# Kernel tuning notes

Measured on AMD Instinct MI355X. Metric: run time of the kernel, lower is better.

The kernel has to match this reference:

```python
import jax, jax.numpy as jnp
import numpy as np

D_MODEL = 1024
N_HEADS = 16
D_HEAD = D_MODEL // N_HEADS
B, T = 2, 2048


def setup_inputs() -> dict:
    key = jax.random.key(0)
    ks = jax.random.split(key, 8)
    s = 1.0 / np.sqrt(D_MODEL)
    return {
        "x": jax.random.normal(ks[0], (B, T, D_MODEL), dtype=jnp.float32),
        "ln_g": jnp.ones((D_MODEL,), jnp.float32),
        "ln_b": jnp.zeros((D_MODEL,), jnp.float32),
        "w_qkv": jax.random.normal(ks[1], (D_MODEL, 3 * D_MODEL), jnp.float32) * s,
        "b_qkv": jnp.zeros((3 * D_MODEL,), jnp.float32),
        "w_gate": jax.random.normal(ks[2], (D_MODEL, D_MODEL), jnp.float32) * s,
        "b_gate": jnp.zeros((D_MODEL,), jnp.float32),
        "w_proj": jax.random.normal(ks[3], (D_MODEL, D_MODEL), jnp.float32) * s,
        "b_proj": jnp.zeros((D_MODEL,), jnp.float32),
    }


def reference(x, ln_g, ln_b, w_qkv, b_qkv, w_gate, b_gate, w_proj, b_proj):
    Bb, Tt, Dd = x.shape
    H, dh = N_HEADS, D_HEAD

    # LayerNorm (eps=1e-5, torch default)
    mu = jnp.mean(x, axis=-1, keepdims=True)
    var = jnp.mean((x - mu) ** 2, axis=-1, keepdims=True)
    x_norm = (x - mu) / jnp.sqrt(var + 1e-5) * ln_g + ln_b

    qkv = x_norm @ w_qkv + b_qkv
    q, k, v = jnp.split(qkv, 3, axis=-1)

    # concept gate on the RAW input x (not x_norm), normalized by its mean
    gate_sig = jax.nn.sigmoid(x @ w_gate + b_gate)
    gate_norm = gate_sig / (jnp.mean(gate_sig, axis=-1, keepdims=True) + 1e-5)
    q = q * gate_norm
    k = k * gate_norm

    # [B,T,D] -> [B,H,T,dh]
    def to_heads(t):
        return t.reshape(Bb, Tt, H, dh).transpose(0, 2, 1, 3)

    q, k, v = to_heads(q), to_heads(k), to_heads(v)

    q = jax.nn.elu(q) + 1.0
    k = jax.nn.elu(k) + 1.0

    # materialized outer-product cumsum (faithful to source formulation)
    kv = jnp.einsum("bhtd,bhtm->bhtdm", k, v)          # [B,H,T,dh,dh]
    kv_cumsum = jnp.cumsum(kv, axis=2)
    out_num = jnp.einsum("bhtd,bhtdm->bhtm", q, kv_cumsum)
    k_cumsum = jnp.cumsum(k, axis=2)
    out_den = jnp.einsum("bhtd,bhtd->bht", q, k_cumsum)[..., None] + 1e-5
    out = out_num / out_den                              # [B,H,T,dh]

    out = out.transpose(0, 2, 1, 3).reshape(Bb, Tt, Dd)
    return out @ w_proj + b_proj
```

## Files before the change

### kernel.cpp

```cpp
#include <hip/hip_runtime.h>
#include <math.h>

constexpr int D      = 1024;
constexpr int H      = 16;
constexpr int DH     = 64;
constexpr int Bb     = 2;
constexpr int T      = 2048;
constexpr int BT     = Bb * T;
constexpr int CHUNK  = 64;
constexpr int NC     = T / CHUNK;
constexpr int LS     = 72;

typedef __attribute__((ext_vector_type(8))) short bf16x8;
typedef __attribute__((ext_vector_type(4))) float f32x4;

#define GLOAD_LDS16(gp, lp) \
    __builtin_amdgcn_global_load_lds((const __attribute__((address_space(1))) void*)(gp), \
                                     (__attribute__((address_space(3))) void*)(lp), 16, 0, 0)

__device__ __forceinline__ short to_bf16(float f) {
    unsigned u = __float_as_uint(f);
    unsigned r = (u + 0x7fffu + ((u >> 16) & 1u)) >> 16;
    return (short)r;
}
__device__ __forceinline__ float bf2f(short s) {
    return __uint_as_float(((unsigned)(unsigned short)s) << 16);
}

__device__ __forceinline__ float elu1(float x) {
    return x > 0.0f ? x + 1.0f : __expf(x);
}

__global__ __launch_bounds__(256) void pre_kernel(const float* __restrict__ x,
                                                  const float* __restrict__ g,
                                                  const float* __restrict__ b,
                                                  const float* __restrict__ wq,
                                                  const float* __restrict__ wg,
                                                  const float* __restrict__ wp,
                                                  short* __restrict__ ynb,
                                                  short* __restrict__ xbb,
                                                  short* __restrict__ wTcomb,
                                                  short* __restrict__ wTp,
                                                  float* __restrict__ gmean) {
    __shared__ short tile[32][33];
    int bid = blockIdx.x;
    if (bid < 1024) {
        int row  = bid * 4 + (threadIdx.x >> 6);
        int lane = threadIdx.x & 63;
        const float* xr = x + (size_t)row * D;
        float4 xv[4];
        float s = 0.0f;
        #pragma unroll
        for (int i = 0; i < 4; ++i) {
            xv[i] = *(const float4*)(xr + i * 256 + lane * 4);
            s += xv[i].x + xv[i].y + xv[i].z + xv[i].w;
        }
        #pragma unroll
        for (int off = 32; off > 0; off >>= 1) s += __shfl_xor(s, off, 64);
        float mu = s * (1.0f / D);
        float vs = 0.0f;
        #pragma unroll
        for (int i = 0; i < 4; ++i) {
            float d0 = xv[i].x - mu, d1 = xv[i].y - mu;
            float d2 = xv[i].z - mu, d3 = xv[i].w - mu;
            vs += d0 * d0 + d1 * d1 + d2 * d2 + d3 * d3;
        }
        #pragma unroll
        for (int off = 32; off > 0; off >>= 1) vs += __shfl_xor(vs, off, 64);
        float rstd = rsqrtf(vs * (1.0f / D) + 1e-5f);
        if (lane == 0) gmean[row] = 0.0f;
        #pragma unroll
        for (int i = 0; i < 4; ++i) {
            int cc = i * 256 + lane * 4;
            float4 gv = *(const float4*)(g + cc);
            float4 bv = *(const float4*)(b + cc);
            short4 o, xo;
            o.x = to_bf16((xv[i].x - mu) * rstd * gv.x + bv.x);
            o.y = to_bf16((xv[i].y - mu) * rstd * gv.y + bv.y);
            o.z = to_bf16((xv[i].z - mu) * rstd * gv.z + bv.z);
            o.w = to_bf16((xv[i].w - mu) * rstd * gv.w + bv.w);
            xo.x = to_bf16(xv[i].x); xo.y = to_bf16(xv[i].y);
            xo.z = to_bf16(xv[i].z); xo.w = to_bf16(xv[i].w);
            *(short4*)(ynb + (size_t)row * D + cc) = o;
            *(short4*)(xbb + (size_t)row * D + cc) = xo;
        }
    } else {
        int t2 = bid - 1024;
        const float* W; short* Wt; int N; int t;
        if (t2 < 3072)      { W = wq; Wt = wTcomb;                       N = 3072; t = t2; }
        else if (t2 < 4096) { W = wg; Wt = wTcomb + (size_t)3072 * 1024; N = 1024; t = t2 - 3072; }
        else                { W = wp; Wt = wTp;                          N = 1024; t = t2 - 4096; }
        int ntiles = N >> 5;
        int nb = (t % ntiles) * 32, kb = (t / ntiles) * 32;
        int tx = threadIdx.x & 31, ty = threadIdx.x >> 5;
        #pragma unroll
        for (int i = 0; i < 4; ++i) {
            int k = kb + ty + i * 8;
            tile[ty + i * 8][tx] = to_bf16(W[(size_t)k * N + nb + tx]);
        }
        __syncthreads();
        #pragma unroll
        for (int i = 0; i < 4; ++i) {
            int n = nb + ty + i * 8;
            Wt[(size_t)n * 1024 + kb + tx] = tile[tx][ty + i * 8];
        }
    }
}

#define SWZ(os) ((os) ^ ((((os) >> 6) & 3) << 3))
#define BARX() __builtin_amdgcn_s_barrier()
#define LGKM0() asm volatile("s_waitcnt lgkmcnt(0)" ::: "memory")
#define VMW(n) asm volatile("s_waitcnt vmcnt(" #n ")" ::: "memory")
#define MEMFENCE() asm volatile("" ::: "memory")

#define STG(Mp, rb, t, kc, isB) do {                                                       \
    short* _b = ldsbuf + ((((t) & 1)) << 15) + (((((isB) << 1) | (kc))) << 13) + wid * 1024; \
    const short* _g = (Mp) + (size_t)((rb) + wid * 32 + s_r) * 1024 + (t) * 64 + (kc) * 32 + s_c; \
    GLOAD_LDS16(_g, _b);                                                                   \
    GLOAD_LDS16(_g + (size_t)16 * 1024, _b + 512);                                         \
} while (0)

#define FRAGA(t, kc, mi) (*(const bf16x8*)(ldsbuf + (((t) & 1) << 15) + ((kc) << 13) + \
    SWZ((wm * 128 + (mi) * 16 + fr) * 32 + fk)))
#define FRAGB(t, kc, ni) (*(const bf16x8*)(ldsbuf + (((t) & 1) << 15) + ((2 + (kc)) << 13) + \
    SWZ((wn * 64 + (ni) * 16 + fr) * 32 + fk)))

#define GROUP(t, S1, S2, S3, S4, W2, W4) do {                                              \
    bf16x8 af[8], bq[4];                                                                   \
    _Pragma("unroll") for (int mi = 0; mi < 8; ++mi) af[mi] = FRAGA(t, 0, mi);             \
// ... 49 lines not shown
                                                             short* __restrict__ sigb,
                                                             float* __restrict__ gmean) {
    __shared__ short ldsbuf[2 * 32768];

    const int bid   = blockIdx.x;
    const int xcd   = bid & 7;
    const int local = bid >> 3;
    const int cx = xcd & 3, ry = xcd >> 2;
    const int bxx = cx * 4 + (local & 3);
    const int byy = ry * 8 + (local >> 2);
    const int row0 = byy * 256;
    const int col0 = bxx * 256;
    const bool isg = (col0 >= 3 * D);
    const short* Ap = isg ? xb : xnb;

    const int tid  = threadIdx.x;
    const int wid  = tid >> 6;
    const int lane = tid & 63;
    const int wm = wid >> 2;
    const int wn = wid & 3;
    const int fr = lane & 15;
    const int fk = (lane >> 4) * 8;

    const int s_r = lane >> 2;
    const int s_c = 8 * ((lane & 3) ^ ((lane >> 3) & 3));

    f32x4 acc[8][4] = {};

    STG(Ap, row0, 0, 0, 0); MEMFENCE();
    STG(Wt, col0, 0, 0, 1); MEMFENCE();
    STG(Ap, row0, 0, 1, 0); MEMFENCE();
    STG(Wt, col0, 0, 1, 1); MEMFENCE();
    STG(Ap, row0, 1, 0, 0); MEMFENCE();
    STG(Wt, col0, 1, 0, 1); MEMFENCE();
    STG(Ap, row0, 1, 1, 0);
    VMW(10);
    BARX();

    for (int t = 0; t < 14; ++t) GROUP(t, 1, 1, 1, 1, VMW(10), VMW(10));
    GROUP(14, 1, 0, 0, 0, VMW(8), VMW(4));
    GROUP(15, 0, 0, 0, 0, VMW(0), (void)0);

    const int ccol  = lane & 15;
    const int crow4 = (lane >> 4) * 4;
    if (!isg) {
        #pragma unroll
        for (int mi = 0; mi < 8; ++mi) {
            #pragma unroll
            for (int ni = 0; ni < 4; ++ni) {
                int col = col0 + wn * 64 + ni * 16 + ccol;
                float bv = b_qkv[col];
                #pragma unroll
                for (int r = 0; r < 4; ++r) {
                    int row = row0 + wm * 128 + mi * 16 + crow4 + r;
                    qkvb[(size_t)row * (3 * D) + col] = to_bf16(acc[mi][ni][r] + bv);
                }
            }
        }
    } else {
        #pragma unroll
        for (int mi = 0; mi < 8; ++mi) {
            #pragma unroll
            for (int r = 0; r < 4; ++r) {
                int lrow = row0 + wm * 128 + mi * 16 + crow4 + r;
                float psum = 0.0f;
                #pragma unroll
                for (int ni = 0; ni < 4; ++ni) {
                    int col = col0 + wn * 64 + ni * 16 + ccol - 3 * D;
                    float v = acc[mi][ni][r] + b_gate[col];
                    float sv = 1.0f / (1.0f + __expf(-v));
                    sigb[(size_t)lrow * D + col] = to_bf16(sv);
                    psum += sv;
                }
                psum += __shfl_xor(psum, 1, 64);
                psum += __shfl_xor(psum, 2, 64);
                psum += __shfl_xor(psum, 4, 64);
                psum += __shfl_xor(psum, 8, 64);
                if (ccol == 0) atomicAdd(&gmean[lrow], psum);
            }
        }
    }
}

__global__ __launch_bounds__(256) void chunk_state_mfma(const short* __restrict__ qkvb,
                                                        const short* __restrict__ sigb,
                                                        const float* __restrict__ gmean,
                                                        float* __restrict__ Sc,
                                                        float* __restrict__ zc) {
    __shared__ short Kt[DH * LS];
    __shared__ short Vt[DH * LS];
    int idx = blockIdx.x;
    int c = idx & (NC - 1), h = (idx >> 5) & (H - 1), b = idx >> 9;
    size_t bt0 = (size_t)b * T + c * CHUNK;
    const short* kbase = qkvb + bt0 * (3 * D) + D + h * DH;
    const short* vbase = kbase + D;
    const short* sbase = sigb + bt0 * D + h * DH;
    int tid = threadIdx.x;

    #pragma unroll
    for (int l = 0; l < 2; ++l) {
        int i  = tid + l * 256;
        int t  = i >> 3;
        int d8 = (i & 7) * 8;
        float invm = 1.0f / (gmean[bt0 + t] * (1.0f / D) + 1e-5f);
        bf16x8 kv = *(const bf16x8*)(kbase + (size_t)t * (3 * D) + d8);
        bf16x8 vv = *(const bf16x8*)(vbase + (size_t)t * (3 * D) + d8);
        bf16x8 sg = *(const bf16x8*)(sbase + (size_t)t * D + d8);
        #pragma unroll
        for (int j = 0; j < 8; ++j) {
            float gn = bf2f(sg[j]) * invm;
            Kt[(d8 + j) * LS + t] = to_bf16(elu1(bf2f(kv[j]) * gn));
            Vt[(d8 + j) * LS + t] = vv[j];
        }
    }
    __syncthreads();

    const int wv = tid >> 6, lane = tid & 63;
    const int fr = lane & 15, quad = lane >> 4;
    const int fk = quad * 8, crow4 = quad * 4, ccol = lane & 15;
    const int mbase = wv * 16;

    bf16x8 af[2];
    af[0] = *(const bf16x8*)&Vt[(mbase + fr) * LS + fk];
    af[1] = *(const bf16x8*)&Vt[(mbase + fr) * LS + 32 + fk];

    f32x4 acc[4] = {};
    #pragma unroll
    for (int n = 0; n < 4; ++n) {
        #pragma unroll
        for (int ck = 0; ck < 2; ++ck) {
            bf16x8 bk = *(const bf16x8*)&Kt[(n * 16 + fr) * LS + ck * 32 + fk];
            acc[n] = __builtin_amdgcn_mfma_f32_16x16x32_bf16(af[ck], bk, acc[n], 0, 0, 0);
        }
    }

    float* Sd = Sc + (size_t)idx * (DH * DH);
    #pragma unroll
    for (int n = 0; n < 4; ++n)
        #pragma unroll
        for (int r = 0; r < 4; ++r)
            Sd[(mbase + crow4 + r) * DH + n * 16 + ccol] = acc[n][r];

    {
        int d = tid >> 2, p = tid & 3;
        bf16x8 k0 = *(const bf16x8*)&Kt[d * LS + p * 16];
        bf16x8 k1 = *(const bf16x8*)&Kt[d * LS + p * 16 + 8];
        float zs = 0.0f;
        #pragma unroll
        for (int j = 0; j < 8; ++j) zs += bf2f(k0[j]) + bf2f(k1[j]);
        zs += __shfl_xor(zs, 1, 64);
        zs += __shfl_xor(zs, 2, 64);
        if (p == 0) zc[(size_t)idx * DH + d] = zs;
    }
}

__global__ __launch_bounds__(256) void chunk_prefix_kernel(const float* __restrict__ S,
                                                           short* __restrict__ Spb,
                                                           float* __restrict__ z) {
    int bh   = blockIdx.x >> 4;
    int part = blockIdx.x & 15;
    int e    = part * 256 + threadIdx.x;
    const float* Sb = S + (size_t)bh * NC * DH * DH;
    short* Pb = Spb + (size_t)bh * NC * DH * DH;
    float v[NC];
    #pragma unroll
    for (int c = 0; c < NC; ++c) v[c] = Sb[(size_t)c * DH * DH + e];
    float acc = 0.0f;
    #pragma unroll
    for (int c = 0; c < NC; ++c) {
        Pb[(size_t)c * DH * DH + e] = to_bf16(acc);
        acc += v[c];
    }
    if (part == 0 && threadIdx.x < DH) {
        float* zb = z + (size_t)bh * NC * DH + threadIdx.x;
        float zv[NC];
        #pragma unroll
        for (int c = 0; c < NC; ++c) zv[c] = zb[(size_t)c * DH];
        float za = 0.0f;
        #pragma unroll
        for (int c = 0; c < NC; ++c) {
            zb[(size_t)c * DH] = za;
            za += zv[c];
        }
    }
}

__global__ __launch_bounds__(256) void chunk_attn_mfma(const short* __restrict__ qkvb,
                                                       const short* __restrict__ sigb,
                                                       const float* __restrict__ gmean,
                                                       const short* __restrict__ Spb,
                                                       const float* __restrict__ zc,
                                                       short* __restrict__ attnb) {
    __shared__ short Qs[CHUNK * LS];
    __shared__ short Ks[CHUNK * LS];
    __shared__ short Vt[DH * LS];
    __shared__ short Ss[DH * LS];
    __shared__ float zpL[DH];
    __shared__ float den[CHUNK];
    short* As = Ks;

    int idx = blockIdx.x;
    int c = idx & (NC - 1), h = (idx >> 5) & (H - 1), b = idx >> 9;
    size_t bt0 = (size_t)b * T + c * CHUNK;
    const short* qbase = qkvb + bt0 * (3 * D) + h * DH;
    const short* kbase = qbase + D;
    const short* vbase = qbase + 2 * D;
    const short* sbase = sigb + bt0 * D + h * DH;
    const short* spb = Spb + (size_t)idx * (DH * DH);
    int tid = threadIdx.x;

    #pragma unroll
    for (int l = 0; l < 2; ++l) {
        int i  = tid + l * 256;
        int t  = i >> 3;
        int d8 = (i & 7) * 8;
        float invm = 1.0f / (gmean[bt0 + t] * (1.0f / D) + 1e-5f);
        bf16x8 qv = *(const bf16x8*)(qbase + (size_t)t * (3 * D) + d8);
        bf16x8 kv = *(const bf16x8*)(kbase + (size_t)t * (3 * D) + d8);
        bf16x8 vv = *(const bf16x8*)(vbase + (size_t)t * (3 * D) + d8);
        bf16x8 sg = *(const bf16x8*)(sbase + (size_t)t * D + d8);
        bf16x8 qg, kg;
        #pragma unroll
        for (int j = 0; j < 8; ++j) {
            float gn = bf2f(sg[j]) * invm;
            qg[j] = to_bf16(elu1(bf2f(qv[j]) * gn));
            kg[j] = to_bf16(elu1(bf2f(kv[j]) * gn));
            Vt[(d8 + j) * LS + t] = vv[j];
        }
        *(bf16x8*)&Qs[t * LS + d8] = qg;
        *(bf16x8*)&Ks[t * LS + d8] = kg;
        *(bf16x8*)&Ss[t * LS + d8] = *(const bf16x8*)(spb + (size_t)i * 8);
    }
    if (tid < DH) zpL[tid] = zc[(size_t)idx * DH + tid];
    __syncthreads();

    const int wv = tid >> 6, lane = tid & 63;
    const int fr = lane & 15, quad = lane >> 4;
    const int fk = quad * 8, crow4 = quad * 4, ccol = lane & 15;
    const int tbase = wv * 16;

    bf16x8 aq[2];
    aq[0] = *(const bf16x8*)&Qs[(tbase + fr) * LS + fk];
    aq[1] = *(const bf16x8*)&Qs[(tbase + fr) * LS + 32 + fk];

    f32x4 accs[4] = {};
    #pragma unroll
    for (int n = 0; n < 4; ++n) {
        #pragma unroll
        for (int ck = 0; ck < 2; ++ck) {
            bf16x8 bk = *(const bf16x8*)&Ks[(n * 16 + fr) * LS + ck * 32 + fk];
            accs[n] = __builtin_amdgcn_mfma_f32_16x16x32_bf16(aq[ck], bk, accs[n], 0, 0, 0);
        }
    }
    __syncthreads();

    float part[4] = {0.f, 0.f, 0.f, 0.f};
    #pragma unroll
    for (int n = 0; n < 4; ++n) {
        #pragma unroll
        for (int r = 0; r < 4; ++r) {
            int tt = tbase + crow4 + r;
            int ss = n * 16 + ccol;
            float v = (ss <= tt) ? accs[n][r] : 0.0f;
            part[r] += v;
            As[tt * LS + ss] = to_bf16(v);
        }
    }
    #pragma unroll
    for (int r = 0; r < 4; ++r) {
        part[r] += __shfl_xor(part[r], 1, 64);
        part[r] += __shfl_xor(part[r], 2, 64);
        part[r] += __shfl_xor(part[r], 4, 64);
        part[r] += __shfl_xor(part[r], 8, 64);
    }
    if (fr == 0) {
        #pragma unroll
        for (int r = 0; r < 4; ++r) den[tbase + crow4 + r] = part[r];
    }
    __syncthreads();

    {
        int t = tid >> 2, p = tid & 3;
        bf16x8 q0 = *(const bf16x8*)&Qs[t * LS + p * 16];
        bf16x8 q1 = *(const bf16x8*)&Qs[t * LS + p * 16 + 8];
        float qz = 0.0f;
        #pragma unroll
        for (int j = 0; j < 8; ++j)
            qz += bf2f(q0[j]) * zpL[p * 16 + j] + bf2f(q1[j]) * zpL[p * 16 + 8 + j];
        qz += __shfl_xor(qz, 1, 64);
        qz += __shfl_xor(qz, 2, 64);
        if (p == 0) den[t] += qz + 1e-5f;
    }

    f32x4 acco[4] = {};
    #pragma unroll
    for (int m4 = 0; m4 < 4; ++m4) {
        #pragma unroll
        for (int ck = 0; ck < 2; ++ck) {
            bf16x8 bs = *(const bf16x8*)&Ss[(m4 * 16 + fr) * LS + ck * 32 + fk];
            acco[m4] = __builtin_amdgcn_mfma_f32_16x16x32_bf16(aq[ck], bs, acco[m4], 0, 0, 0);
        }
    }
    bf16x8 aa[2];
    aa[0] = *(const bf16x8*)&As[(tbase + fr) * LS + fk];
    aa[1] = *(const bf16x8*)&As[(tbase + fr) * LS + 32 + fk];
    #pragma unroll
    for (int m4 = 0; m4 < 4; ++m4) {
        #pragma unroll
        for (int ck = 0; ck < 2; ++ck) {
            bf16x8 bv = *(const bf16x8*)&Vt[(m4 * 16 + fr) * LS + ck * 32 + fk];
            acco[m4] = __builtin_amdgcn_mfma_f32_16x16x32_bf16(aa[ck], bv, acco[m4], 0, 0, 0);
        }
    }
    __syncthreads();

    short* obase = attnb + bt0 * D + h * DH;
    #pragma unroll
    for (int r = 0; r < 4; ++r) {
        int tt = tbase + crow4 + r;
        float rv = 1.0f / den[tt];
        #pragma unroll
        for (int m4 = 0; m4 < 4; ++m4)
            obase[(size_t)tt * D + m4 * 16 + ccol] = to_bf16(acco[m4][r] * rv);
    }
}

__global__ __launch_bounds__(256) void gemm_proj64(const short* __restrict__ A,
                                                   const short* __restrict__ Bt,
                                                   const float* __restrict__ bias,
                                                   float* __restrict__ C) {
    constexpr int BK = 32, K = 1024, N = 1024;
    __shared__ short Als[64 * BK];
    __shared__ short Bls[128 * BK];

    const int bid   = blockIdx.x;
    const int xcd   = bid & 7;
    const int local = bid >> 3;
    const int cx = xcd & 3, ry = xcd >> 2;
    const int lx = local & 1, ly = local >> 1;
    const int bxx = cx * 2 + lx;
    const int byy = ry * 32 + ly;

    const int tid  = threadIdx.x;
    const int wave = tid >> 6;
    const int lane = tid & 63;
    const int row0 = byy * 64;
    const int col0 = bxx * 128;
    const int wn = wave * 32;

    f32x4 acc[4][2] = {};
    const int srow = lane >> 2;
    const int skk  = (lane & 3) * 8;
    const int fr = lane & 15;
    const int fk = (lane >> 4) * 8;

    for (int k0 = 0; k0 < K; k0 += BK) {
        __syncthreads();
        #pragma unroll
        for (int u = 0; u < 3; ++u) {
            int cc = wave * 3 + u;
            if (cc < 4) {
                int r = cc * 16 + srow;
                GLOAD_LDS16(A + (size_t)(row0 + r) * K + k0 + skk, &Als[cc * 512]);
            } else {
                int c2 = cc - 4;
                int r = c2 * 16 + srow;
                GLOAD_LDS16(Bt + (size_t)(col0 + r) * K + k0 + skk, &Bls[c2 * 512]);
            }
        }
        __syncthreads();

        bf16x8 af[4], bfr[2];
        #pragma unroll
        for (int i = 0; i < 4; ++i)
            af[i] = *(const bf16x8*)&Als[(i * 16 + fr) * BK + fk];
        #pragma unroll
        for (int j = 0; j < 2; ++j)
            bfr[j] = *(const bf16x8*)&Bls[(wn + j * 16 + fr) * BK + fk];
        #pragma unroll
        for (int mi = 0; mi < 4; ++mi)
            #pragma unroll
            for (int ni = 0; ni < 2; ++ni)
                acc[mi][ni] = __builtin_amdgcn_mfma_f32_16x16x32_bf16(af[mi], bfr[ni], acc[mi][ni], 0, 0, 0);
    }

    const int ccol  = lane & 15;
    const int crow4 = (lane >> 4) * 4;
    #pragma unroll
    for (int mi = 0; mi < 4; ++mi) {
        #pragma unroll
        for (int ni = 0; ni < 2; ++ni) {
            int col = col0 + wn + ni * 16 + ccol;
            float bv = bias[col];
            #pragma unroll
            for (int r = 0; r < 4; ++r) {
                int row = row0 + mi * 16 + crow4 + r;
                C[(size_t)row * N + col] = acc[mi][ni][r] + bv;
            }
        }
    }
}

extern "C" void kernel_launch(void* const* d_in, const int* in_sizes, int n_in,
                              void* d_out, int out_size, void* d_ws, size_t ws_size,
                              hipStream_t stream) {
    const float* x      = (const float*)d_in[0];
    const float* ln_g   = (const float*)d_in[1];
    const float* ln_b   = (const float*)d_in[2];
    const float* w_qkv  = (const float*)d_in[3];
    const float* b_qkv  = (const float*)d_in[4];
    const float* w_gate = (const float*)d_in[5];
    const float* b_gate = (const float*)d_in[6];
    const float* w_proj = (const float*)d_in[7];
    const float* b_proj = (const float*)d_in[8];
    float* out = (float*)d_out;

    short* xnb   = (short*)d_ws;
    short* xb    = xnb + (size_t)BT * D;
    short* wTc   = xb + (size_t)BT * D;
    short* wTp   = wTc + (size_t)4096 * 1024;
    short* qkvb  = wTp + (size_t)D * D;
    short* sigb  = qkvb + (size_t)BT * 3 * D;
    short* attnb = sigb + (size_t)BT * D;
    float* zc    = (float*)(attnb + (size_t)BT * D);
    float* gmean = zc + (size_t)Bb * H * NC * DH;
    float* Sc    = (float*)xnb;
    short* Spb   = wTc;

    pre_kernel<<<1024 + 5120, 256, 0, stream>>>(x, ln_g, ln_b, w_qkv, w_gate, w_proj,
                                                xnb, xb, wTc, wTp, gmean);
    gemm_fused_qkvgate<<<256, 512, 0, stream>>>(
        xnb, xb, wTc, b_qkv, b_gate, qkvb, sigb, gmean);
    chunk_state_mfma<<<Bb * H * NC, 256, 0, stream>>>(qkvb, sigb, gmean, Sc, zc);
    chunk_prefix_kernel<<<Bb * H * 16, 256, 0, stream>>>(Sc, Spb, zc);
    chunk_attn_mfma<<<Bb * H * NC, 256, 0, stream>>>(qkvb, sigb, gmean, Spb, zc, attnb);
    gemm_proj64<<<512, 256, 0, stream>>>(attnb, wTp, b_proj, out);
}
```

Before: 190.6 us.

## Fuse chunk state, prefix and attention kernels with software grid barriers

Merges the three chunked linear-attention kernels into one persistent 512-block kernel, with two atomic-counter grid barriers replacing the kernel boundaries. Each block handles two chunks and keeps their transposed V tiles in LDS across the barriers, so V is not reloaded in the attention phase. The aim is to cut two launch gaps and some global traffic. The cost is that all 512 blocks must be co-resident (launch bounds request 3 blocks per CU) or the barrier deadlocks, and LDS use per block grows.

```diff
diff --git a/kernel.cpp b/kernel.cpp
--- a/kernel.cpp
+++ b/kernel.cpp
@@ -29,6 +29,17 @@
 
 __device__ __forceinline__ float elu1(float x) {
     return x > 0.0f ? x + 1.0f : __expf(x);
+}
+
+__device__ __forceinline__ void grid_barrier(unsigned* ctr, unsigned target) {
+    __threadfence();
+    __syncthreads();
+    if (threadIdx.x == 0) {
+        __hip_atomic_fetch_add(ctr, 1u, __ATOMIC_ACQ_REL, __HIP_MEMORY_SCOPE_AGENT);
+        while (__hip_atomic_load(ctr, __ATOMIC_ACQUIRE, __HIP_MEMORY_SCOPE_AGENT) < target)
+            __builtin_amdgcn_s_sleep(2);
+    }
+    __syncthreads();
 }
 
 __global__ __launch_bounds__(256) void pre_kernel(const float* __restrict__ x,
@@ -41,10 +52,12 @@
                                                   short* __restrict__ xbb,
                                                   short* __restrict__ wTcomb,
                                                   short* __restrict__ wTp,
-                                                  float* __restrict__ gmean) {
+                                                  float* __restrict__ gmean,
+                                                  unsigned* __restrict__ ctrs) {
     __shared__ short tile[32][33];
     int bid = blockIdx.x;
     if (bid < 1024) {
+        if (bid == 0 && threadIdx.x < 2) ctrs[threadIdx.x] = 0;
         int row  = bid * 4 + (threadIdx.x >> 6);
         int lane = threadIdx.x & 63;
         const float* xr = x + (size_t)row * D;
@@ -260,246 +273,240 @@
     }
 }
 
-__global__ __launch_bounds__(256) void chunk_state_mfma(const short* __restrict__ qkvb,
-                                                        const short* __restrict__ sigb,
-                                                        const float* __restrict__ gmean,
-                                                        float* __restrict__ Sc,
-                                                        float* __restrict__ zc) {
-    __shared__ short Kt[DH * LS];
-    __shared__ short Vt[DH * LS];
-    int idx = blockIdx.x;
-    int c = idx & (NC - 1), h = (idx >> 5) & (H - 1), b = idx >> 9;
-    size_t bt0 = (size_t)b * T + c * CHUNK;
-    const short* kbase = qkvb + bt0 * (3 * D) + D + h * DH;
-    const short* vbase = kbase + D;
-    const short* sbase = sigb + bt0 * D + h * DH;
-    int tid = threadIdx.x;
-
-    #pragma unroll
-    for (int l = 0; l < 2; ++l) {
-        int i  = tid + l * 256;
-        int t  = i >> 3;
-        int d8 = (i & 7) * 8;
-        float invm = 1.0f / (gmean[bt0 + t] * (1.0f / D) + 1e-5f);
-        bf16x8 kv = *(const bf16x8*)(kbase + (size_t)t * (3 * D) + d8);
-        bf16x8 vv = *(const bf16x8*)(vbase + (size_t)t * (3 * D) + d8);
-        bf16x8 sg = *(const bf16x8*)(sbase + (size_t)t * D + d8);
-        #pragma unroll
-        for (int j = 0; j < 8; ++j) {
-            float gn = bf2f(sg[j]) * invm;
-            Kt[(d8 + j) * LS + t] = to_bf16(elu1(bf2f(kv[j]) * gn));
-            Vt[(d8 + j) * LS + t] = vv[j];
-        }
-    }
-    __syncthreads();
-
-    const int wv = tid >> 6, lane = tid & 63;
-    const int fr = lane & 15, quad = lane >> 4;
-    const int fk = quad * 8, crow4 = quad * 4, ccol = lane & 15;
-    const int mbase = wv * 16;
-
-    bf16x8 af[2];
-    af[0] = *(const bf16x8*)&Vt[(mbase + fr) * LS + fk];
-    af[1] = *(const bf16x8*)&Vt[(mbase + fr) * LS + 32 + fk];
-
-    f32x4 acc[4] = {};
-    #pragma unroll
-    for (int n = 0; n < 4; ++n) {
-        #pragma unroll
-        for (int ck = 0; ck < 2; ++ck) {
-            bf16x8 bk = *(const bf16x8*)&Kt[(n * 16 + fr) * LS + ck * 32 + fk];
-            acc[n] = __builtin_amdgcn_mfma_f32_16x16x32_bf16(af[ck], bk, acc[n], 0, 0, 0);
-        }
-    }
-
-    float* Sd = Sc + (size_t)idx * (DH * DH);
-    #pragma unroll
-    for (int n = 0; n < 4; ++n)
-        #pragma unroll
-        for (int r = 0; r < 4; ++r)
-            Sd[(mbase + crow4 + r) * DH + n * 16 + ccol] = acc[n][r];
-
-    {
-        int d = tid >> 2, p = tid & 3;
-        bf16x8 k0 = *(const bf16x8*)&Kt[d * LS + p * 16];
-        bf16x8 k1 = *(const bf16x8*)&Kt[d * LS + p * 16 + 8];
-        float zs = 0.0f;
-        #pragma unroll
-        for (int j = 0; j < 8; ++j) zs += bf2f(k0[j]) + bf2f(k1[j]);
-        zs += __shfl_xor(zs, 1, 64);
-        zs += __shfl_xor(zs, 2, 64);
-        if (p == 0) zc[(size_t)idx * DH + d] = zs;
-    }
-}
-
-__global__ __launch_bounds__(256) void chunk_prefix_kernel(const float* __restrict__ S,
-                                                           short* __restrict__ Spb,
-                                                           float* __restrict__ z) {
-    int bh   = blockIdx.x >> 4;
-    int part = blockIdx.x & 15;
-    int e    = part * 256 + threadIdx.x;
-    const float* Sb = S + (size_t)bh * NC * DH * DH;
-    short* Pb = Spb + (size_t)bh * NC * DH * DH;
-    float v[NC];
-    #pragma unroll
-    for (int c = 0; c < NC; ++c) v[c] = Sb[(size_t)c * DH * DH + e];
-    float acc = 0.0f;
-    #pragma unroll
-    for (int c = 0; c < NC; ++c) {
-        Pb[(size_t)c * DH * DH + e] = to_bf16(acc);
-        acc += v[c];
-    }
-    if (part == 0 && threadIdx.x < DH) {
-        float* zb = z + (size_t)bh * NC * DH + threadIdx.x;
-        float zv[NC];
-        #pragma unroll
-        for (int c = 0; c < NC; ++c) zv[c] = zb[(size_t)c * DH];
-        float za = 0.0f;
-        #pragma unroll
-        for (int c = 0; c < NC; ++c) {
-            zb[(size_t)c * DH] = za;
-            za += zv[c];
-        }
-    }
-}
-
-__global__ __launch_bounds__(256) void chunk_attn_mfma(const short* __restrict__ qkvb,
-                                                       const short* __restrict__ sigb,
-                                                       const float* __restrict__ gmean,
-                                                       const short* __restrict__ Spb,
-                                                       const float* __restrict__ zc,
-                                                       short* __restrict__ attnb) {
+__global__ __launch_bounds__(256, 3) void chunk_fused(const short* __restrict__ qkvb,
+                                                      const short* __restrict__ sigb,
+                                                      const float* __restrict__ gmean,
+                                                      float* __restrict__ Sc,
+                                                      short* __restrict__ Spb,
+                                                      float* __restrict__ zc,
+                                                      short* __restrict__ attnb,
+                                                      unsigned* __restrict__ ctrs) {
     __shared__ short Qs[CHUNK * LS];
     __shared__ short Ks[CHUNK * LS];
-    __shared__ short Vt[DH * LS];
+    __shared__ short VtA[DH * LS];
+    __shared__ short VtB[DH * LS];
     __shared__ short Ss[DH * LS];
     __shared__ float zpL[DH];
     __shared__ float den[CHUNK];
     short* As = Ks;
 
-    int idx = blockIdx.x;
-    int c = idx & (NC - 1), h = (idx >> 5) & (H - 1), b = idx >> 9;
-    size_t bt0 = (size_t)b * T + c * CHUNK;
-    const short* qbase = qkvb + bt0 * (3 * D) + h * DH;
-    const short* kbase = qbase + D;
-    const short* vbase = qbase + 2 * D;
-    const short* sbase = sigb + bt0 * D + h * DH;
-    const short* spb = Spb + (size_t)idx * (DH * DH);
-    int tid = threadIdx.x;
-
-    #pragma unroll
-    for (int l = 0; l < 2; ++l) {
-        int i  = tid + l * 256;
-        int t  = i >> 3;
-        int d8 = (i & 7) * 8;
-        float invm = 1.0f / (gmean[bt0 + t] * (1.0f / D) + 1e-5f);
-        bf16x8 qv = *(const bf16x8*)(qbase + (size_t)t * (3 * D) + d8);
-        bf16x8 kv = *(const bf16x8*)(kbase + (size_t)t * (3 * D) + d8);
-        bf16x8 vv = *(const bf16x8*)(vbase + (size_t)t * (3 * D) + d8);
-        bf16x8 sg = *(const bf16x8*)(sbase + (size_t)t * D + d8);
-        bf16x8 qg, kg;
-        #pragma unroll
-        for (int j = 0; j < 8; ++j) {
-            float gn = bf2f(sg[j]) * invm;
-            qg[j] = to_bf16(elu1(bf2f(qv[j]) * gn));
-            kg[j] = to_bf16(elu1(bf2f(kv[j]) * gn));
-            Vt[(d8 + j) * LS + t] = vv[j];
-        }
-        *(bf16x8*)&Qs[t * LS + d8] = qg;
-        *(bf16x8*)&Ks[t * LS + d8] = kg;
-        *(bf16x8*)&Ss[t * LS + d8] = *(const bf16x8*)(spb + (size_t)i * 8);
-    }
-    if (tid < DH) zpL[tid] = zc[(size_t)idx * DH + tid];
-    __syncthreads();
-
+    const int bid = blockIdx.x;
+    const int tid = threadIdx.x;
     const int wv = tid >> 6, lane = tid & 63;
     const int fr = lane & 15, quad = lane >> 4;
     const int fk = quad * 8, crow4 = quad * 4, ccol = lane & 15;
-    const int tbase = wv * 16;
-
-    bf16x8 aq[2];
-    aq[0] = *(const bf16x8*)&Qs[(tbase + fr) * LS + fk];
-    aq[1] = *(const bf16x8*)&Qs[(tbase + fr) * LS + 32 + fk];
-
-    f32x4 accs[4] = {};
+
     #pragma unroll
-    for (int n = 0; n < 4; ++n) {
-        #pragma unroll
-        for (int ck = 0; ck < 2; ++ck) {
-            bf16x8 bk = *(const bf16x8*)&Ks[(n * 16 + fr) * LS + ck * 32 + fk];
-            accs[n] = __builtin_amdgcn_mfma_f32_16x16x32_bf16(aq[ck], bk, accs[n], 0, 0, 0);
-        }
-    }
-    __syncthreads();
-
-    float part[4] = {0.f, 0.f, 0.f, 0.f};
+    for (int half = 0; half < 2; ++half) {
+        if (half) __syncthreads();
+        int idx = bid * 2 + half;
+        int c = idx & (NC - 1), h = (idx >> 5) & (H - 1), b = idx >> 9;
+        size_t bt0 = (size_t)b * T + c * CHUNK;
+        const short* kbase = qkvb + bt0 * (3 * D) + D + h * DH;
+        const short* vbase = kbase + D;
+        const short* sbase = sigb + bt0 * D + h * DH;
+        short* Kt = Qs;
+        short* Vt = half ? VtB : VtA;
+
+        #pragma unroll
+        for (int l = 0; l < 2; ++l) {
+            int i  = tid + l * 256;
+            int t  = i >> 3;
+            int d8 = (i & 7) * 8;
+            float invm = 1.0f / (gmean[bt0 + t] * (1.0f / D) + 1e-5f);
+            bf16x8 kv = *(const bf16x8*)(kbase + (size_t)t * (3 * D) + d8);
+            bf16x8 vv = *(const bf16x8*)(vbase + (size_t)t * (3 * D) + d8);
+            bf16x8 sg = *(const bf16x8*)(sbase + (size_t)t * D + d8);
+            #pragma unroll
+            for (int j = 0; j < 8; ++j) {
+                float gn = bf2f(sg[j]) * invm;
+                Kt[(d8 + j) * LS + t] = to_bf16(elu1(bf2f(kv[j]) * gn));
+                Vt[(d8 + j) * LS + t] = vv[j];
+            }
+        }
+        __syncthreads();
+
+        const int mbase = wv * 16;
+        bf16x8 af0 = *(const bf16x8*)&Vt[(mbase + fr) * LS + fk];
+        bf16x8 af1 = *(const bf16x8*)&Vt[(mbase + fr) * LS + 32 + fk];
+
+        f32x4 acc[4] = {};
+        #pragma unroll
+        for (int n = 0; n < 4; ++n) {
+            bf16x8 bk0 = *(const bf16x8*)&Kt[(n * 16 + fr) * LS + fk];
+            bf16x8 bk1 = *(const bf16x8*)&Kt[(n * 16 + fr) * LS + 32 + fk];
+            acc[n] = __builtin_amdgcn_mfma_f32_16x16x32_bf16(af0, bk0, acc[n], 0, 0, 0);
+            acc[n] = __builtin_amdgcn_mfma_f32_16x16x32_bf16(af1, bk1, acc[n], 0, 0, 0);
+        }
+
+        float* Sd = Sc + (size_t)idx * (DH * DH);
+        #pragma unroll
+        for (int n = 0; n < 4; ++n)
+            #pragma unroll
+            for (int r = 0; r < 4; ++r)
+                Sd[(mbase + crow4 + r) * DH + n * 16 + ccol] = acc[n][r];
+
+        {
+            int d = tid >> 2, p = tid & 3;
+            bf16x8 k0 = *(const bf16x8*)&Kt[d * LS + p * 16];
+            bf16x8 k1 = *(const bf16x8*)&Kt[d * LS + p * 16 + 8];
+            float zs = 0.0f;
+            #pragma unroll
+            for (int j = 0; j < 8; ++j) zs += bf2f(k0[j]) + bf2f(k1[j]);
+            zs += __shfl_xor(zs, 1, 64);
+            zs += __shfl_xor(zs, 2, 64);
+            if (p == 0) zc[(size_t)idx * DH + d] = zs;
+        }
+    }
+
+    grid_barrier(&ctrs[0], 512);
+
+    {
+        int bh = bid >> 4, part = bid & 15;
+        int e = part * 256 + tid;
+        const float* Sb = Sc + (size_t)bh * NC * DH * DH;
+        short* Pb = Spb + (size_t)bh * NC * DH * DH;
+        float v[NC];
+        #pragma unroll
+        for (int cc = 0; cc < NC; ++cc) v[cc] = Sb[(size_t)cc * DH * DH + e];
+        float pacc = 0.0f;
+        #pragma unroll
+        for (int cc = 0; cc < NC; ++cc) {
+            Pb[(size_t)cc * DH * DH + e] = to_bf16(pacc);
+            pacc += v[cc];
+        }
+        if (part == 0 && tid < DH) {
+            float* zb = zc + (size_t)bh * NC * DH + tid;
+            float zv[NC];
+            #pragma unroll
+            for (int cc = 0; cc < NC; ++cc) zv[cc] = zb[(size_t)cc * DH];
+            float za = 0.0f;
+            #pragma unroll
+            for (int cc = 0; cc < NC; ++cc) {
+                zb[(size_t)cc * DH] = za;
+                za += zv[cc];
+            }
+        }
+    }
+
+    grid_barrier(&ctrs[1], 512);
+
     #pragma unroll
-    for (int n = 0; n < 4; ++n) {
+    for (int half = 0; half < 2; ++half) {
+        __syncthreads();
+        int idx = bid * 2 + half;
+        int c = idx & (NC - 1), h = (idx >> 5) & (H - 1), b = idx >> 9;
+        size_t bt0 = (size_t)b * T + c * CHUNK;
+        const short* qbase = qkvb + bt0 * (3 * D) + h * DH;
+        const short* kbase = qbase + D;
+        const short* sbase = sigb + bt0 * D + h * DH;
+        const short* spb = Spb + (size_t)idx * (DH * DH);
+        const short* Vt = half ? VtB : VtA;
+
+        #pragma unroll
+        for (int l = 0; l < 2; ++l) {
+            int i  = tid + l * 256;
+            int t  = i >> 3;
+            int d8 = (i & 7) * 8;
+            float invm = 1.0f / (gmean[bt0 + t] * (1.0f / D) + 1e-5f);
+            bf16x8 qv = *(const bf16x8*)(qbase + (size_t)t * (3 * D) + d8);
+            bf16x8 kv = *(const bf16x8*)(kbase + (size_t)t * (3 * D) + d8);
+            bf16x8 sg = *(const bf16x8*)(sbase + (size_t)t * D + d8);
+            bf16x8 qg, kg;
+            #pragma unroll
+            for (int j = 0; j < 8; ++j) {
+                float gn = bf2f(sg[j]) * invm;
+                qg[j] = to_bf16(elu1(bf2f(qv[j]) * gn));
+                kg[j] = to_bf16(elu1(bf2f(kv[j]) * gn));
+            }
+            *(bf16x8*)&Qs[t * LS + d8] = qg;
+            *(bf16x8*)&Ks[t * LS + d8] = kg;
+            *(bf16x8*)&Ss[t * LS + d8] = *(const bf16x8*)(spb + (size_t)i * 8);
+        }
+        if (tid < DH) zpL[tid] = zc[(size_t)idx * DH + tid];
+        __syncthreads();
+
+        const int tbase = wv * 16;
+
+        bf16x8 aq0 = *(const bf16x8*)&Qs[(tbase + fr) * LS + fk];
+        bf16x8 aq1 = *(const bf16x8*)&Qs[(tbase + fr) * LS + 32 + fk];
+
+        f32x4 accs[4] = {};
+        #pragma unroll
+        for (int n = 0; n < 4; ++n) {
+            bf16x8 bk0 = *(const bf16x8*)&Ks[(n * 16 + fr) * LS + fk];
+            bf16x8 bk1 = *(const bf16x8*)&Ks[(n * 16 + fr) * LS + 32 + fk];
+            accs[n] = __builtin_amdgcn_mfma_f32_16x16x32_bf16(aq0, bk0, accs[n], 0, 0, 0);
+            accs[n] = __builtin_amdgcn_mfma_f32_16x16x32_bf16(aq1, bk1, accs[n], 0, 0, 0);
+        }
+        __syncthreads();
+
+        float part[4] = {0.f, 0.f, 0.f, 0.f};
+        #pragma unroll
+        for (int n = 0; n < 4; ++n) {
+            #pragma unroll
+            for (int r = 0; r < 4; ++r) {
+                int tt = tbase + crow4 + r;
+                int ss = n * 16 + ccol;
+                float v = (ss <= tt) ? accs[n][r] : 0.0f;
+                part[r] += v;
+                As[tt * LS + ss] = to_bf16(v);
+            }
+        }
+        #pragma unroll
+        for (int r = 0; r < 4; ++r) {
+            part[r] += __shfl_xor(part[r], 1, 64);
+            part[r] += __shfl_xor(part[r], 2, 64);
+            part[r] += __shfl_xor(part[r], 4, 64);
+            part[r] += __shfl_xor(part[r], 8, 64);
+        }
+        if (fr == 0) {
+            #pragma unroll
+            for (int r = 0; r < 4; ++r) den[tbase + crow4 + r] = part[r];
+        }
+        __syncthreads();
+
+        {
+            int t = tid >> 2, p = tid & 3;
+            bf16x8 q0 = *(const bf16x8*)&Qs[t * LS + p * 16];
+            bf16x8 q1 = *(const bf16x8*)&Qs[t * LS + p * 16 + 8];
+            float qz = 0.0f;
+            #pragma unroll
+            for (int j = 0; j < 8; ++j)
+                qz += bf2f(q0[j]) * zpL[p * 16 + j] + bf2f(q1[j]) * zpL[p * 16 + 8 + j];
+            qz += __shfl_xor(qz, 1, 64);
+            qz += __shfl_xor(qz, 2, 64);
+            if (p == 0) den[t] += qz + 1e-5f;
+        }
+
+        f32x4 acco[4] = {};
+        #pragma unroll
+        for (int m4 = 0; m4 < 4; ++m4) {
+            bf16x8 bs0 = *(const bf16x8*)&Ss[(m4 * 16 + fr) * LS + fk];
+            bf16x8 bs1 = *(const bf16x8*)&Ss[(m4 * 16 + fr) * LS + 32 + fk];
+            acco[m4] = __builtin_amdgcn_mfma_f32_16x16x32_bf16(aq0, bs0, acco[m4], 0, 0, 0);
+            acco[m4] = __builtin_amdgcn_mfma_f32_16x16x32_bf16(aq1, bs1, acco[m4], 0, 0, 0);
+        }
+        bf16x8 aa0 = *(const bf16x8*)&As[(tbase + fr) * LS + fk];
+        bf16x8 aa1 = *(const bf16x8*)&As[(tbase + fr) * LS + 32 + fk];
+        #pragma unroll
+        for (int m4 = 0; m4 < 4; ++m4) {
+            bf16x8 bv0 = *(const bf16x8*)&Vt[(m4 * 16 + fr) * LS + fk];
+            bf16x8 bv1 = *(const bf16x8*)&Vt[(m4 * 16 + fr) * LS + 32 + fk];
+            acco[m4] = __builtin_amdgcn_mfma_f32_16x16x32_bf16(aa0, bv0, acco[m4], 0, 0, 0);
+            acco[m4] = __builtin_amdgcn_mfma_f32_16x16x32_bf16(aa1, bv1, acco[m4], 0, 0, 0);
+        }
+        __syncthreads();
+
+        short* obase = attnb + bt0 * D + h * DH;
         #pragma unroll
         for (int r = 0; r < 4; ++r) {
             int tt = tbase + crow4 + r;
-            int ss = n * 16 + ccol;
-            float v = (ss <= tt) ? accs[n][r] : 0.0f;
-            part[r] += v;
-            As[tt * LS + ss] = to_bf16(v);
-        }
-    }
-    #pragma unroll
-    for (int r = 0; r < 4; ++r) {
-        part[r] += __shfl_xor(part[r], 1, 64);
-        part[r] += __shfl_xor(part[r], 2, 64);
-        part[r] += __shfl_xor(part[r], 4, 64);
-        part[r] += __shfl_xor(part[r], 8, 64);
-    }
-    if (fr == 0) {
-        #pragma unroll
-        for (int r = 0; r < 4; ++r) den[tbase + crow4 + r] = part[r];
-    }
-    __syncthreads();
-
-    {
-        int t = tid >> 2, p = tid & 3;
-        bf16x8 q0 = *(const bf16x8*)&Qs[t * LS + p * 16];
-        bf16x8 q1 = *(const bf16x8*)&Qs[t * LS + p * 16 + 8];
-        float qz = 0.0f;
-        #pragma unroll
-        for (int j = 0; j < 8; ++j)
-            qz += bf2f(q0[j]) * zpL[p * 16 + j] + bf2f(q1[j]) * zpL[p * 16 + 8 + j];
-        qz += __shfl_xor(qz, 1, 64);
-        qz += __shfl_xor(qz, 2, 64);
-        if (p == 0) den[t] += qz + 1e-5f;
-    }
-
-    f32x4 acco[4] = {};
-    #pragma unroll
-    for (int m4 = 0; m4 < 4; ++m4) {
-        #pragma unroll
-        for (int ck = 0; ck < 2; ++ck) {
-            bf16x8 bs = *(const bf16x8*)&Ss[(m4 * 16 + fr) * LS + ck * 32 + fk];
-            acco[m4] = __builtin_amdgcn_mfma_f32_16x16x32_bf16(aq[ck], bs, acco[m4], 0, 0, 0);
-        }
-    }
-    bf16x8 aa[2];
-    aa[0] = *(const bf16x8*)&As[(tbase + fr) * LS + fk];
-    aa[1] = *(const bf16x8*)&As[(tbase + fr) * LS + 32 + fk];
-    #pragma unroll
-    for (int m4 = 0; m4 < 4; ++m4) {
-        #pragma unroll
-        for (int ck = 0; ck < 2; ++ck) {
-            bf16x8 bv = *(const bf16x8*)&Vt[(m4 * 16 + fr) * LS + ck * 32 + fk];
-            acco[m4] = __builtin_amdgcn_mfma_f32_16x16x32_bf16(aa[ck], bv, acco[m4], 0, 0, 0);
-        }
-    }
-    __syncthreads();
-
-    short* obase = attnb + bt0 * D + h * DH;
-    #pragma unroll
-    for (int r = 0; r < 4; ++r) {
-        int tt = tbase + crow4 + r;
-        float rv = 1.0f / den[tt];
-        #pragma unroll
-        for (int m4 = 0; m4 < 4; ++m4)
-            obase[(size_t)tt * D + m4 * 16 + ccol] = to_bf16(acco[m4][r] * rv);
+            float rv = 1.0f / den[tt];
+            #pragma unroll
+            for (int m4 = 0; m4 < 4; ++m4)
+                obase[(size_t)tt * D + m4 * 16 + ccol] = to_bf16(acco[m4][r] * rv);
+        }
     }
 }
 
@@ -602,15 +609,14 @@
     short* attnb = sigb + (size_t)BT * D;
     float* zc    = (float*)(attnb + (size_t)BT * D);
     float* gmean = zc + (size_t)Bb * H * NC * DH;
+    unsigned* ctrs = (unsigned*)(gmean + BT);
     float* Sc    = (float*)xnb;
     short* Spb   = wTc;
 
     pre_kernel<<<1024 + 5120, 256, 0, stream>>>(x, ln_g, ln_b, w_qkv, w_gate, w_proj,
-                                                xnb, xb, wTc, wTp, gmean);
+                                                xnb, xb, wTc, wTp, gmean, ctrs);
     gemm_fused_qkvgate<<<256, 512, 0, stream>>>(
         xnb, xb, wTc, b_qkv, b_gate, qkvb, sigb, gmean);
-    chunk_state_mfma<<<Bb * H * NC, 256, 0, stream>>>(qkvb, sigb, gmean, Sc, zc);
-    chunk_prefix_kernel<<<Bb * H * 16, 256, 0, stream>>>(Sc, Spb, zc);
-    chunk_attn_mfma<<<Bb * H * NC, 256, 0, stream>>>(qkvb, sigb, gmean, Spb, zc, attnb);
+    chunk_fused<<<512, 256, 0, stream>>>(qkvb, sigb, gmean, Sc, Spb, zc, attnb, ctrs);
     gemm_proj64<<<512, 256, 0, stream>>>(attnb, wTp, b_proj, out);
 }
```

New measurement: 377.3 us. 1.98x slower.

## Fold chunk prefix sum into attention kernel and widen projection GEMM K tile

Applied to the files above, without the earlier changes.

Removes the separate chunk_prefix kernel. Each attention block now sums all earlier per-chunk KV states and z vectors straight from the fp32 Sc buffer, converting to bf16 in LDS. This saves a launch and a bf16 round-trip buffer, but adds redundant O(c) global reads per block that grow with chunk index. Separately, the projection GEMM moves to BK=64 with an XOR-swizzled LDS layout to cut bank conflicts and halve barrier count. The LDS row stride changes from 72 to 70 shorts, which breaks 16-byte alignment of the vector LDS accesses.

```diff
diff --git a/kernel.cpp b/kernel.cpp
--- a/kernel.cpp
+++ b/kernel.cpp
@@ -9,7 +9,7 @@
 constexpr int BT     = Bb * T;
 constexpr int CHUNK  = 64;
 constexpr int NC     = T / CHUNK;
-constexpr int LS     = 72;
+constexpr int LS     = 70;
 
 typedef __attribute__((ext_vector_type(8))) short bf16x8;
 typedef __attribute__((ext_vector_type(4))) float f32x4;
@@ -30,6 +30,7 @@
 __device__ __forceinline__ float elu1(float x) {
     return x > 0.0f ? x + 1.0f : __expf(x);
 }
+
 
 __global__ __launch_bounds__(256) void pre_kernel(const float* __restrict__ x,
                                                   const float* __restrict__ g,
@@ -298,18 +299,16 @@
     const int fk = quad * 8, crow4 = quad * 4, ccol = lane & 15;
     const int mbase = wv * 16;
 
-    bf16x8 af[2];
-    af[0] = *(const bf16x8*)&Vt[(mbase + fr) * LS + fk];
-    af[1] = *(const bf16x8*)&Vt[(mbase + fr) * LS + 32 + fk];
+    bf16x8 af0 = *(const bf16x8*)&Vt[(mbase + fr) * LS + fk];
+    bf16x8 af1 = *(const bf16x8*)&Vt[(mbase + fr) * LS + 32 + fk];
 
     f32x4 acc[4] = {};
     #pragma unroll
     for (int n = 0; n < 4; ++n) {
-        #pragma unroll
-        for (int ck = 0; ck < 2; ++ck) {
-            bf16x8 bk = *(const bf16x8*)&Kt[(n * 16 + fr) * LS + ck * 32 + fk];
-            acc[n] = __builtin_amdgcn_mfma_f32_16x16x32_bf16(af[ck], bk, acc[n], 0, 0, 0);
-        }
+        bf16x8 bk0 = *(const bf16x8*)&Kt[(n * 16 + fr) * LS + fk];
+        bf16x8 bk1 = *(const bf16x8*)&Kt[(n * 16 + fr) * LS + 32 + fk];
+        acc[n] = __builtin_amdgcn_mfma_f32_16x16x32_bf16(af0, bk0, acc[n], 0, 0, 0);
+        acc[n] = __builtin_amdgcn_mfma_f32_16x16x32_bf16(af1, bk1, acc[n], 0, 0, 0);
     }
 
     float* Sd = Sc + (size_t)idx * (DH * DH);
@@ -332,41 +331,10 @@
     }
 }
 
-__global__ __launch_bounds__(256) void chunk_prefix_kernel(const float* __restrict__ S,
-                                                           short* __restrict__ Spb,
-                                                           float* __restrict__ z) {
-    int bh   = blockIdx.x >> 4;
-    int part = blockIdx.x & 15;
-    int e    = part * 256 + threadIdx.x;
-    const float* Sb = S + (size_t)bh * NC * DH * DH;
-    short* Pb = Spb + (size_t)bh * NC * DH * DH;
-    float v[NC];
-    #pragma unroll
-    for (int c = 0; c < NC; ++c) v[c] = Sb[(size_t)c * DH * DH + e];
-    float acc = 0.0f;
-    #pragma unroll
-    for (int c = 0; c < NC; ++c) {
-        Pb[(size_t)c * DH * DH + e] = to_bf16(acc);
-        acc += v[c];
-    }
-    if (part == 0 && threadIdx.x < DH) {
-        float* zb = z + (size_t)bh * NC * DH + threadIdx.x;
-        float zv[NC];
-        #pragma unroll
-        for (int c = 0; c < NC; ++c) zv[c] = zb[(size_t)c * DH];
-        float za = 0.0f;
-        #pragma unroll
-        for (int c = 0; c < NC; ++c) {
-            zb[(size_t)c * DH] = za;
-            za += zv[c];
-        }
-    }
-}
-
 __global__ __launch_bounds__(256) void chunk_attn_mfma(const short* __restrict__ qkvb,
                                                        const short* __restrict__ sigb,
                                                        const float* __restrict__ gmean,
-                                                       const short* __restrict__ Spb,
+                                                       const float* __restrict__ Sc,
                                                        const float* __restrict__ zc,
                                                        short* __restrict__ attnb) {
     __shared__ short Qs[CHUNK * LS];
@@ -384,7 +352,6 @@
     const short* kbase = qbase + D;
     const short* vbase = qbase + 2 * D;
     const short* sbase = sigb + bt0 * D + h * DH;
-    const short* spb = Spb + (size_t)idx * (DH * DH);
     int tid = threadIdx.x;
 
     #pragma unroll
@@ -407,9 +374,33 @@
         }
         *(bf16x8*)&Qs[t * LS + d8] = qg;
         *(bf16x8*)&Ks[t * LS + d8] = kg;
-        *(bf16x8*)&Ss[t * LS + d8] = *(const bf16x8*)(spb + (size_t)i * 8);
-    }
-    if (tid < DH) zpL[tid] = zc[(size_t)idx * DH + tid];
+    }
+
+    {
+        const float* Sb = Sc + (size_t)(idx & ~(NC - 1)) * (DH * DH) + tid * 16;
+        f32x4 a0 = {}, a1 = {}, a2 = {}, a3 = {};
+        for (int cc = 0; cc < c; ++cc) {
+            const float* p = Sb + (size_t)cc * (DH * DH);
+            a0 += *(const f32x4*)(p);
+            a1 += *(const f32x4*)(p + 4);
+            a2 += *(const f32x4*)(p + 8);
+            a3 += *(const f32x4*)(p + 12);
+        }
+        int m = tid >> 2, d0 = (tid & 3) * 16;
+        bf16x8 s0, s1;
+        #pragma unroll
+        for (int j = 0; j < 4; ++j) { s0[j] = to_bf16(a0[j]); s0[4 + j] = to_bf16(a1[j]); }
+        #pragma unroll
+        for (int j = 0; j < 4; ++j) { s1[j] = to_bf16(a2[j]); s1[4 + j] = to_bf16(a3[j]); }
+        *(bf16x8*)&Ss[m * LS + d0]     = s0;
+        *(bf16x8*)&Ss[m * LS + d0 + 8] = s1;
+    }
+    if (tid < DH) {
+        const float* zb = zc + (size_t)(idx & ~(NC - 1)) * DH + tid;
+        float zp = 0.0f;
+        for (int cc = 0; cc < c; ++cc) zp += zb[(size_t)cc * DH];
+        zpL[tid] = zp;
+    }
     __syncthreads();
 
     const int wv = tid >> 6, lane = tid & 63;
@@ -417,18 +408,16 @@
     const int fk = quad * 8, crow4 = quad * 4, ccol = lane & 15;
     const int tbase = wv * 16;
 
-    bf16x8 aq[2];
-    aq[0] = *(const bf16x8*)&Qs[(tbase + fr) * LS + fk];
-    aq[1] = *(const bf16x8*)&Qs[(tbase + fr) * LS + 32 + fk];
+    bf16x8 aq0 = *(const bf16x8*)&Qs[(tbase + fr) * LS + fk];
+    bf16x8 aq1 = *(const bf16x8*)&Qs[(tbase + fr) * LS + 32 + fk];
 
     f32x4 accs[4] = {};
     #pragma unroll
     for (int n = 0; n < 4; ++n) {
-        #pragma unroll
-        for (int ck = 0; ck < 2; ++ck) {
-            bf16x8 bk = *(const bf16x8*)&Ks[(n * 16 + fr) * LS + ck * 32 + fk];
-            accs[n] = __builtin_amdgcn_mfma_f32_16x16x32_bf16(aq[ck], bk, accs[n], 0, 0, 0);
-        }
+        bf16x8 bk0 = *(const bf16x8*)&Ks[(n * 16 + fr) * LS + fk];
+        bf16x8 bk1 = *(const bf16x8*)&Ks[(n * 16 + fr) * LS + 32 + fk];
+        accs[n] = __builtin_amdgcn_mfma_f32_16x16x32_bf16(aq0, bk0, accs[n], 0, 0, 0);
+        accs[n] = __builtin_amdgcn_mfma_f32_16x16x32_bf16(aq1, bk1, accs[n], 0, 0, 0);
     }
     __syncthreads();
 
@@ -473,22 +462,19 @@
     f32x4 acco[4] = {};
     #pragma unroll
     for (int m4 = 0; m4 < 4; ++m4) {
-        #pragma unroll
-        for (int ck = 0; ck < 2; ++ck) {
-            bf16x8 bs = *(const bf16x8*)&Ss[(m4 * 16 + fr) * LS + ck * 32 + fk];
-            acco[m4] = __builtin_amdgcn_mfma_f32_16x16x32_bf16(aq[ck], bs, acco[m4], 0, 0, 0);
-        }
-    }
-    bf16x8 aa[2];
-    aa[0] = *(const bf16x8*)&As[(tbase + fr) * LS + fk];
-    aa[1] = *(const bf16x8*)&As[(tbase + fr) * LS + 32 + fk];
+        bf16x8 bs0 = *(const bf16x8*)&Ss[(m4 * 16 + fr) * LS + fk];
+        bf16x8 bs1 = *(const bf16x8*)&Ss[(m4 * 16 + fr) * LS + 32 + fk];
+        acco[m4] = __builtin_amdgcn_mfma_f32_16x16x32_bf16(aq0, bs0, acco[m4], 0, 0, 0);
+        acco[m4] = __builtin_amdgcn_mfma_f32_16x16x32_bf16(aq1, bs1, acco[m4], 0, 0, 0);
+    }
+    bf16x8 aa0 = *(const bf16x8*)&As[(tbase + fr) * LS + fk];
+    bf16x8 aa1 = *(const bf16x8*)&As[(tbase + fr) * LS + 32 + fk];
     #pragma unroll
     for (int m4 = 0; m4 < 4; ++m4) {
-        #pragma unroll
-        for (int ck = 0; ck < 2; ++ck) {
-            bf16x8 bv = *(const bf16x8*)&Vt[(m4 * 16 + fr) * LS + ck * 32 + fk];
-            acco[m4] = __builtin_amdgcn_mfma_f32_16x16x32_bf16(aa[ck], bv, acco[m4], 0, 0, 0);
-        }
+        bf16x8 bv0 = *(const bf16x8*)&Vt[(m4 * 16 + fr) * LS + fk];
+        bf16x8 bv1 = *(const bf16x8*)&Vt[(m4 * 16 + fr) * LS + 32 + fk];
+        acco[m4] = __builtin_amdgcn_mfma_f32_16x16x32_bf16(aa0, bv0, acco[m4], 0, 0, 0);
+        acco[m4] = __builtin_amdgcn_mfma_f32_16x16x32_bf16(aa1, bv1, acco[m4], 0, 0, 0);
     }
     __syncthreads();
 
@@ -502,12 +488,15 @@
             obase[(size_t)tt * D + m4 * 16 + ccol] = to_bf16(acco[m4][r] * rv);
     }
 }
+
+#define SWZ64(os) ((os) ^ ((((os) >> 6) & 7) << 3))
 
 __global__ __launch_bounds__(256) void gemm_proj64(const short* __restrict__ A,
                                                    const short* __restrict__ Bt,
                                                    const float* __restrict__ bias,
                                                    float* __restrict__ C) {
-    constexpr int BK = 32, K = 1024, N = 1024;
+    constexpr int BK = 64, K = 1024;
+    constexpr int N = 1024;
     __shared__ short Als[64 * BK];
     __shared__ short Bls[128 * BK];
 
@@ -527,39 +516,40 @@
     const int wn = wave * 32;
 
     f32x4 acc[4][2] = {};
-    const int srow = lane >> 2;
-    const int skk  = (lane & 3) * 8;
     const int fr = lane & 15;
     const int fk = (lane >> 4) * 8;
 
     for (int k0 = 0; k0 < K; k0 += BK) {
         __syncthreads();
         #pragma unroll
-        for (int u = 0; u < 3; ++u) {
-            int cc = wave * 3 + u;
-            if (cc < 4) {
-                int r = cc * 16 + srow;
-                GLOAD_LDS16(A + (size_t)(row0 + r) * K + k0 + skk, &Als[cc * 512]);
-            } else {
-                int c2 = cc - 4;
-                int r = c2 * 16 + srow;
-                GLOAD_LDS16(Bt + (size_t)(col0 + r) * K + k0 + skk, &Bls[c2 * 512]);
-            }
+        for (int u = 0; u < 2; ++u) {
+            int slot = tid + u * 256;
+            int r = slot >> 3, c8 = (slot & 7) ^ (r & 7);
+            GLOAD_LDS16(A + (size_t)(row0 + r) * K + k0 + c8 * 8, &Als[slot * 8]);
+        }
+        #pragma unroll
+        for (int u = 0; u < 4; ++u) {
+            int slot = tid + u * 256;
+            int r = slot >> 3, c8 = (slot & 7) ^ (r & 7);
+            GLOAD_LDS16(Bt + (size_t)(col0 + r) * K + k0 + c8 * 8, &Bls[slot * 8]);
         }
         __syncthreads();
 
-        bf16x8 af[4], bfr[2];
-        #pragma unroll
-        for (int i = 0; i < 4; ++i)
-            af[i] = *(const bf16x8*)&Als[(i * 16 + fr) * BK + fk];
-        #pragma unroll
-        for (int j = 0; j < 2; ++j)
-            bfr[j] = *(const bf16x8*)&Bls[(wn + j * 16 + fr) * BK + fk];
-        #pragma unroll
-        for (int mi = 0; mi < 4; ++mi)
+        #pragma unroll
+        for (int ck = 0; ck < 2; ++ck) {
+            bf16x8 af[4], bfr[2];
             #pragma unroll
-            for (int ni = 0; ni < 2; ++ni)
-                acc[mi][ni] = __builtin_amdgcn_mfma_f32_16x16x32_bf16(af[mi], bfr[ni], acc[mi][ni], 0, 0, 0);
+            for (int i = 0; i < 4; ++i)
+                af[i] = *(const bf16x8*)&Als[SWZ64((i * 16 + fr) * BK + ck * 32 + fk)];
+            #pragma unroll
+            for (int j = 0; j < 2; ++j)
+                bfr[j] = *(const bf16x8*)&Bls[SWZ64((wn + j * 16 + fr) * BK + ck * 32 + fk)];
+            #pragma unroll
+            for (int mi = 0; mi < 4; ++mi)
+                #pragma unroll
+                for (int ni = 0; ni < 2; ++ni)
+                    acc[mi][ni] = __builtin_amdgcn_mfma_f32_16x16x32_bf16(af[mi], bfr[ni], acc[mi][ni], 0, 0, 0);
+        }
     }
 
     const int ccol  = lane & 15;
@@ -603,14 +593,12 @@
     float* zc    = (float*)(attnb + (size_t)BT * D);
     float* gmean = zc + (size_t)Bb * H * NC * DH;
     float* Sc    = (float*)xnb;
-    short* Spb   = wTc;
 
     pre_kernel<<<1024 + 5120, 256, 0, stream>>>(x, ln_g, ln_b, w_qkv, w_gate, w_proj,
                                                 xnb, xb, wTc, wTp, gmean);
     gemm_fused_qkvgate<<<256, 512, 0, stream>>>(
         xnb, xb, wTc, b_qkv, b_gate, qkvb, sigb, gmean);
     chunk_state_mfma<<<Bb * H * NC, 256, 0, stream>>>(qkvb, sigb, gmean, Sc, zc);
-    chunk_prefix_kernel<<<Bb * H * 16, 256, 0, stream>>>(Sc, Spb, zc);
-    chunk_attn_mfma<<<Bb * H * NC, 256, 0, stream>>>(qkvb, sigb, gmean, Spb, zc, attnb);
+    chunk_attn_mfma<<<Bb * H * NC, 256, 0, stream>>>(qkvb, sigb, gmean, Sc, zc, attnb);
     gemm_proj64<<<512, 256, 0, stream>>>(attnb, wTp, b_proj, out);
 }
```

New measurement: 204.5 us. +7.3%, slower.
